# Optimization experiments

Measured on AMD Instinct MI355X. Metric: run time of the kernel, lower is better.

The kernel has to match this reference:

```python
import jax, jax.numpy as jnp
import numpy as np

N_WAY = 5
NKPTS = 17
EMBED = 512
N_SUPPORT = 25  # 5-way 5-shot
N_QUERY = 65536


def setup_inputs() -> dict:
    key = jax.random.key(0)
    ks = jax.random.split(key, 12)
    def lin(k, fan_in, fan_out):
        return jax.random.normal(k, (fan_in, fan_out), jnp.float32) / np.float32(np.sqrt(fan_in))
    return {
        'support_features': jax.random.normal(ks[0], (1, N_SUPPORT, EMBED), jnp.float32),
        'support_keypoints': jax.random.uniform(ks[1], (N_SUPPORT, NKPTS, 2), jnp.float32),
        'query_features': jax.random.normal(ks[2], (N_QUERY, EMBED), jnp.float32),
        'image_coords': jax.random.uniform(ks[3], (N_QUERY, 2), jnp.float32) * 512.0,
        'W1': lin(ks[4], EMBED, EMBED), 'b1': jnp.zeros((EMBED,), jnp.float32),
        'W2': lin(ks[5], EMBED, EMBED), 'b2': jnp.zeros((EMBED,), jnp.float32),
        'Wo1': lin(ks[6], EMBED, EMBED // 2), 'bo1': jnp.zeros((EMBED // 2,), jnp.float32),
        'Wo2': lin(ks[7], EMBED // 2, 2), 'bo2': jnp.zeros((2,), jnp.float32),
        'Wc1': lin(ks[8], EMBED, EMBED // 2), 'bc1': jnp.zeros((EMBED // 2,), jnp.float32),
        'Wc2': lin(ks[9], EMBED // 2, 1), 'bc2': jnp.zeros((1,), jnp.float32),
        'temperature': jnp.float32(1.0),
    }


def reference(support_features, support_keypoints, query_features, image_coords,
              W1, b1, W2, b2, Wo1, bo1, Wo2, bo2, Wc1, bc1, Wc2, bc2, temperature):
    eps = 1e-8
    nkpts = support_keypoints.shape[1]
    n_query = query_features.shape[0]
    D = query_features.shape[-1]

    # --- compute_prototypes (batch_size == 1; per-kpt prototype identical by construction) ---
    sf = support_features.reshape(-1, D)                      # [Ns, D]
    h = jnp.maximum(sf @ W1 + b1, 0.0) @ W2 + b2              # prototype_net MLP
    n_per = h.shape[0] // N_WAY
    proto_way = h.reshape(N_WAY, n_per, D).mean(axis=1)       # [n_way, D]
    prototypes = jnp.broadcast_to(proto_way[:, None, :], (N_WAY, nkpts, D))

    # --- compute_distances: 1 - cosine_sim, scaled by temperature ---
    qn = jnp.linalg.norm(query_features, axis=-1)             # [Nq]
    pn = jnp.linalg.norm(proto_way, axis=-1)                  # [n_way]
    sim = (query_features @ proto_way.T) / jnp.maximum(qn[:, None] * pn[None, :], eps)
    dist_way = (1.0 - sim) / temperature                      # [Nq, n_way]
    distances = jnp.broadcast_to(dist_way[:, :, None], (n_query, N_WAY, nkpts))

    # --- predict_keypoints ---
    # avg over kpts is a no-op (identical per kpt); argmin over ways
    class_predictions = jnp.argmin(dist_way, axis=1)          # [Nq] int
    # softmax over a single scalar == 1.0, so keypoints == offset broadcast over kpts
    offset = jnp.maximum(query_features @ Wo1 + bo1, 0.0) @ Wo2 + bo2   # [Nq, 2]
    conf = jax.nn.sigmoid(jnp.maximum(query_features @ Wc1 + bc1, 0.0) @ Wc2 + bc2)  # [Nq, 1]
    keypoints = jnp.broadcast_to(offset[:, None, :], (n_query, nkpts, 2))
    keypoints = jax.nn.sigmoid(keypoints) * image_coords[:, None, :]    # image_coords provided
    confidence = jnp.broadcast_to(conf, (n_query, nkpts))

    return keypoints, confidence, distances, class_predictions, prototypes
```

## Files before the change

### kernel.cpp

```cpp
#include <hip/hip_runtime.h>
#include <hip/hip_bf16.h>

#define NQ 65536
#define DIM 512
#define HID 256
#define NWAY 5
#define NKPTS 17
#define NS 25

typedef short bf16x8 __attribute__((ext_vector_type(8)));
typedef float f32x4 __attribute__((ext_vector_type(4)));
typedef _Float16 half8 __attribute__((ext_vector_type(8)));

static __device__ __forceinline__ unsigned short f2bf(float f) {
    unsigned int x = __float_as_uint(f);
    unsigned int r = (x + 0x7fffu + ((x >> 16) & 1u)) >> 16;
    return (unsigned short)r;
}

__global__ __launch_bounds__(256) void k_sup(const float* __restrict__ in,
                                             const float* __restrict__ W, const float* __restrict__ b,
                                             float* __restrict__ out, int relu) {
    int w = blockIdx.x * 4 + (threadIdx.x >> 6);
    int lane = threadIdx.x & 63;
    int s = w >> 9;
    int c = w & 511;
    const float* ip = in + s * DIM + lane * 8;
    float4 a0 = *(const float4*)ip;
    float4 a1 = *(const float4*)(ip + 4);
    float av[8] = {a0.x, a0.y, a0.z, a0.w, a1.x, a1.y, a1.z, a1.w};
    float acc = 0.0f;
    #pragma unroll
    for (int j = 0; j < 8; j++)
        acc += av[j] * W[(lane * 8 + j) * DIM + c];
    #pragma unroll
    for (int off = 32; off > 0; off >>= 1)
        acc += __shfl_xor(acc, off, 64);
    if (lane == 0) {
        float v = acc + b[c];
        out[s * DIM + c] = relu ? fmaxf(v, 0.0f) : v;
    }
}

__global__ __launch_bounds__(256) void k_proto(const float* __restrict__ ws_h,
                                               float* __restrict__ ws_proto, float* __restrict__ ws_pn,
                                               float* __restrict__ out_proto) {
    int w = blockIdx.x, t = threadIdx.x;
    __shared__ float s_p[DIM];
    __shared__ float red[256];
    for (int i = t; i < DIM; i += 256) {
        float a = 0.0f;
        for (int s = 0; s < 5; s++) a += ws_h[(w * 5 + s) * DIM + i];
        a *= 0.2f;
        s_p[i] = a;
        ws_proto[w * DIM + i] = a;
    }
    __syncthreads();
    float qq = 0.0f;
    for (int i = t; i < DIM; i += 256) qq += s_p[i] * s_p[i];
    red[t] = qq;
    __syncthreads();
    for (int s2 = 128; s2 > 0; s2 >>= 1) {
        if (t < s2) red[t] += red[t + s2];
        __syncthreads();
    }
    if (t == 0) ws_pn[w] = sqrtf(red[0]);
    for (int i = t; i < NKPTS * DIM; i += 256)
        out_proto[(size_t)w * NKPTS * DIM + i] = s_p[i & (DIM - 1)];
}

__global__ __launch_bounds__(256) void k_convw(const float* __restrict__ Wo1, const float* __restrict__ Wc1,
                                               unsigned short* __restrict__ wb) {
    int c = blockIdx.x;
    const float* src = (c < 256) ? Wo1 : Wc1;
    int cc = (c < 256) ? c : (c - 256);
    for (int k = threadIdx.x; k < DIM; k += 256)
        wb[c * DIM + k] = f2bf(src[k * HID + cc]);
}

__global__ __launch_bounds__(256, 2) void k_fused(const float* __restrict__ qf, const unsigned short* __restrict__ wb,
                                                  const float* __restrict__ ws_proto, const float* __restrict__ ws_pn,
                                                  const float* __restrict__ temp_p,
                                                  const float* __restrict__ bo1, const float* __restrict__ Wo2,
                                                  const float* __restrict__ bo2,
                                                  const float* __restrict__ bc1, const float* __restrict__ Wc2,
                                                  const float* __restrict__ bc2,
                                                  const float* __restrict__ ic,
                                                  float* __restrict__ out_kp, float* __restrict__ out_conf,
                                                  float* __restrict__ out_dist, float* __restrict__ out_class) {
    __shared__ __align__(16) char smem[37120];
    unsigned short* Alds = (unsigned short*)smem;
    unsigned short* Blds = (unsigned short*)(smem + 5120);
    float* s_proto = (float*)(smem + 25600);
    float* dlds = (float*)(smem + 35840);
    _Float16* hlds = (_Float16*)smem;
    float* offlds = (float*)(smem + 33792);

    int bx = blockIdx.x;
    int mb = bx >> 1;
    int nb = bx & 1;
    int t = threadIdx.x;
    int wv = t >> 6;
    int lane = t & 63;
    int r = lane & 15;
    int q8 = (lane >> 4) * 8;

    f32x4 acc[4][4];
    #pragma unroll
    for (int i = 0; i < 4; i++)
        #pragma unroll
        for (int j = 0; j < 4; j++) {
            f32x4 z = {0.0f, 0.0f, 0.0f, 0.0f};
            acc[i][j] = z;
        }

    int am = t >> 2;
    int akc = t & 3;
    const float* aptr = qf + ((size_t)(mb * 64 + am)) * DIM + akc * 8;
    const unsigned short* bptr = wb + ((size_t)(nb * 256 + t)) * DIM;

    if (nb == 0)
        for (int i = t; i < NWAY * DIM; i += 256) s_proto[i] = ws_proto[i];

    float ds[NWAY] = {0, 0, 0, 0, 0};
    float qq = 0.0f;

    float4 A0 = *(const float4*)(aptr);
    float4 A1 = *(const float4*)(aptr + 4);
    uint4 B0 = *(const uint4*)(bptr);
    uint4 B1 = *(const uint4*)(bptr + 8);
    uint4 B2 = *(const uint4*)(bptr + 16);
    uint4 B3 = *(const uint4*)(bptr + 24);

    for (int it = 0; it < 16; it++) {
        unsigned int p0 = f2bf(A0.x) | ((unsigned int)f2bf(A0.y) << 16);
        unsigned int p1 = f2bf(A0.z) | ((unsigned int)f2bf(A0.w) << 16);
        unsigned int p2 = f2bf(A1.x) | ((unsigned int)f2bf(A1.y) << 16);
        unsigned int p3 = f2bf(A1.z) | ((unsigned int)f2bf(A1.w) << 16);
        float av[8] = {A0.x, A0.y, A0.z, A0.w, A1.x, A1.y, A1.z, A1.w};
        __syncthreads();
        *(uint4*)(Alds + am * 40 + akc * 8) = make_uint4(p0, p1, p2, p3);
        *(uint4*)(Blds + t * 40) = B0;
        *(uint4*)(Blds + t * 40 + 8) = B1;
        *(uint4*)(Blds + t * 40 + 16) = B2;
        *(uint4*)(Blds + t * 40 + 24) = B3;
        __syncthreads();
        if (it < 15) {
            int k1 = (it + 1) * 32;
            A0 = *(const float4*)(aptr + k1);
            A1 = *(const float4*)(aptr + k1 + 4);
            B0 = *(const uint4*)(bptr + k1);
            B1 = *(const uint4*)(bptr + k1 + 8);
            B2 = *(const uint4*)(bptr + k1 + 16);
            B3 = *(const uint4*)(bptr + k1 + 24);
        }
        if (nb == 0) {
            int kb = it * 32 + akc * 8;
            #pragma unroll
            for (int w = 0; w < NWAY; w++) {
                f32x4 pv0 = *(const f32x4*)(s_proto + w * DIM + kb);
                f32x4 pv1 = *(const f32x4*)(s_proto + w * DIM + kb + 4);
                ds[w] += av[0] * pv0[0] + av[1] * pv0[1] + av[2] * pv0[2] + av[3] * pv0[3]
                       + av[4] * pv1[0] + av[5] * pv1[1] + av[6] * pv1[2] + av[7] * pv1[3];
            }
            #pragma unroll
            for (int j = 0; j < 8; j++) qq += av[j] * av[j];
        }
        bf16x8 af[4], bf[4];
        #pragma unroll
        for (int mt = 0; mt < 4; mt++)
            af[mt] = *(const bf16x8*)(Alds + (mt * 16 + r) * 40 + q8);
        #pragma unroll
        for (int nt = 0; nt < 4; nt++)
            bf[nt] = *(const bf16x8*)(Blds + (wv * 64 + nt * 16 + r) * 40 + q8);
        #pragma unroll
        for (int mt = 0; mt < 4; mt++)
            #pragma unroll
            for (int nt = 0; nt < 4; nt++)
                acc[mt][nt] = __builtin_amdgcn_mfma_f32_16x16x32_bf16(af[mt], bf[nt], acc[mt][nt], 0, 0, 0);
    }

    if (nb == 0) {
        #pragma unroll
        for (int off = 1; off <= 2; off <<= 1) {
            #pragma unroll
            for (int w = 0; w < NWAY; w++) ds[w] += __shfl_xor(ds[w], off, 64);
            qq += __shfl_xor(qq, off, 64);
        }
        if (akc == 0) {
            float qn = sqrtf(qq);
            float invt = 1.0f / temp_p[0];
            float mv = 1e30f;
            int ami = 0;
            #pragma unroll
            for (int w = 0; w < NWAY; w++) {
                float den = fmaxf(qn * ws_pn[w], 1e-8f);
                float d = (1.0f - ds[w] / den) * invt;
                dlds[am * 5 + w] = d;
                if (d < mv) { mv = d; ami = w; }
            }
            out_class[mb * 64 + am] = (float)ami;
        }
    }
    __syncthreads();
    if (nb == 0) {
        for (int i = t; i < 64 * NWAY * NKPTS; i += 256) {
            int q = i / (NWAY * NKPTS);
            int rem = i - q * (NWAY * NKPTS);
            out_dist[(size_t)(mb * 64 + q) * (NWAY * NKPTS) + rem] = dlds[q * 5 + rem / NKPTS];
        }
    }

    const float* bias = nb ? bc1 : bo1;
    #pragma unroll
    for (int nt = 0; nt < 4; nt++) {
        int cl = wv * 64 + nt * 16 + r;
        float bv = bias[cl];
        #pragma unroll
        for (int mt = 0; mt < 4; mt++)
            #pragma unroll
            for (int rg = 0; rg < 4; rg++) {
                int ml = mt * 16 + (lane >> 4) * 4 + rg;
                float v = acc[mt][nt][rg] + bv;
                hlds[ml * 264 + cl] = (_Float16)fmaxf(v, 0.0f);
            }
    }
    __syncthreads();

    if (nb == 0) {
        if (t < 64) {
            float ox = bo2[0], oy = bo2[1];
            for (int c0 = 0; c0 < 256; c0 += 8) {
                half8 hv = *(const half8*)(hlds + t * 264 + c0);
                #pragma unroll
                for (int j = 0; j < 8; j++) {
                    float hf = (float)hv[j];
                    ox += hf * Wo2[(c0 + j) * 2];
                    oy += hf * Wo2[(c0 + j) * 2 + 1];
                }
            }
            offlds[t * 2] = ox;
            offlds[t * 2 + 1] = oy;
        }
        __syncthreads();
        for (int i = t; i < 64 * 34; i += 256) {
            int q = i / 34;
            int rem = i - q * 34;
            int j = rem & 1;
            size_t Q = (size_t)mb * 64 + q;
            float o = offlds[q * 2 + j];
            float sg = 1.0f / (1.0f + __expf(-o));
            out_kp[Q * 34 + rem] = sg * ic[Q * 2 + j];
        }
    } else {
        if (t < 64) {
            float cl2 = bc2[0];
            for (int c0 = 0; c0 < 256; c0 += 8) {
                half8 hv = *(const half8*)(hlds + t * 264 + c0);
                #pragma unroll
                for (int j = 0; j < 8; j++) cl2 += (float)hv[j] * Wc2[c0 + j];
            }
            offlds[t] = 1.0f / (1.0f + __expf(-cl2));
        }
        __syncthreads();
        for (int i = t; i < 64 * 17; i += 256) {
            int q = i / 17;
            out_conf[(size_t)mb * 64 * 17 + i] = offlds[q];
        }
    }
}

extern "C" void kernel_launch(void* const* d_in, const int* in_sizes, int n_in,
                              void* d_out, int out_size, void* d_ws, size_t ws_size,
                              hipStream_t stream) {
    const float* sf = (const float*)d_in[0];
    const float* qf = (const float*)d_in[2];
    const float* ic = (const float*)d_in[3];
    const float* W1 = (const float*)d_in[4];
    const float* b1 = (const float*)d_in[5];
    const float* W2 = (const float*)d_in[6];
    const float* b2 = (const float*)d_in[7];
    const float* Wo1 = (const float*)d_in[8];
    const float* bo1 = (const float*)d_in[9];
    const float* Wo2 = (const float*)d_in[10];
    const float* bo2 = (const float*)d_in[11];
    const float* Wc1 = (const float*)d_in[12];
    const float* bc1 = (const float*)d_in[13];
    const float* Wc2 = (const float*)d_in[14];
    const float* bc2 = (const float*)d_in[15];
    const float* temp = (const float*)d_in[16];

    float* out = (float*)d_out;
    float* out_kp = out;
    float* out_conf = out + 2228224;
    float* out_dist = out + 3342336;
    float* out_class = out + 8912896;
    float* out_proto = out + 8978432;

    char* ws = (char*)d_ws;
    float* ws_h = (float*)ws;
    float* ws_proto = (float*)(ws + 51200);
    float* ws_pn = (float*)(ws + 61440);
    unsigned short* ws_wb = (unsigned short*)(ws + 65536);
    float* ws_h1 = (float*)(ws + 589824);

    hipLaunchKernelGGL(k_sup, dim3(3200), dim3(256), 0, stream, sf, W1, b1, ws_h1, 1);
    hipLaunchKernelGGL(k_sup, dim3(3200), dim3(256), 0, stream, ws_h1, W2, b2, ws_h, 0);
    hipLaunchKernelGGL(k_proto, dim3(5), dim3(256), 0, stream, ws_h, ws_proto, ws_pn, out_proto);
    hipLaunchKernelGGL(k_convw, dim3(512), dim3(256), 0, stream, Wo1, Wc1, ws_wb);
    hipLaunchKernelGGL(k_fused, dim3(2048), dim3(256), 0, stream, qf, ws_wb, ws_proto, ws_pn, temp,
                       bo1, Wo2, bo2, bc1, Wc2, bc2, ic, out_kp, out_conf, out_dist, out_class);
}
```

Measured before the change: 395.5 us.

## Fuse prototype mean into second support GEMM and split cosine work across blocks

Averages the support hidden activations before applying W2, using linearity, so the second support layer runs on 5 rows instead of 25. That layer is merged with a tiled LDS transpose/bf16 conversion of Wo1/Wc1 into one kernel, which cuts launches from five to three. The prototype-norm and prototype-broadcast kernel is removed: norms are recomputed inside the fused kernel and the prototype output is written by its first blocks. Cosine-distance work and distance output writes are now split between the two column blocks instead of all landing on nb==0. The launch_bounds occupancy hint of 2 is dropped, which may change register allocation.

```diff
diff --git a/kernel.cpp b/kernel.cpp
--- a/kernel.cpp
+++ b/kernel.cpp
@@ -6,7 +6,6 @@
 #define HID 256
 #define NWAY 5
 #define NKPTS 17
-#define NS 25
 
 typedef short bf16x8 __attribute__((ext_vector_type(8)));
 typedef float f32x4 __attribute__((ext_vector_type(4)));
@@ -18,81 +17,104 @@
     return (unsigned short)r;
 }
 
-__global__ __launch_bounds__(256) void k_sup(const float* __restrict__ in,
-                                             const float* __restrict__ W, const float* __restrict__ b,
-                                             float* __restrict__ out, int relu) {
+__global__ __launch_bounds__(256) void k_sup1(const float* __restrict__ sf,
+                                              const float* __restrict__ W1, const float* __restrict__ b1,
+                                              float* __restrict__ ws_h1) {
     int w = blockIdx.x * 4 + (threadIdx.x >> 6);
     int lane = threadIdx.x & 63;
     int s = w >> 9;
     int c = w & 511;
-    const float* ip = in + s * DIM + lane * 8;
+    const float* ip = sf + s * DIM + lane * 8;
     float4 a0 = *(const float4*)ip;
     float4 a1 = *(const float4*)(ip + 4);
     float av[8] = {a0.x, a0.y, a0.z, a0.w, a1.x, a1.y, a1.z, a1.w};
     float acc = 0.0f;
     #pragma unroll
     for (int j = 0; j < 8; j++)
-        acc += av[j] * W[(lane * 8 + j) * DIM + c];
+        acc += av[j] * W1[(lane * 8 + j) * DIM + c];
     #pragma unroll
     for (int off = 32; off > 0; off >>= 1)
         acc += __shfl_xor(acc, off, 64);
-    if (lane == 0) {
-        float v = acc + b[c];
-        out[s * DIM + c] = relu ? fmaxf(v, 0.0f) : v;
-    }
-}
-
-__global__ __launch_bounds__(256) void k_proto(const float* __restrict__ ws_h,
-                                               float* __restrict__ ws_proto, float* __restrict__ ws_pn,
+    if (lane == 0)
+        ws_h1[s * DIM + c] = fmaxf(acc + b1[c], 0.0f);
+}
+
+__global__ __launch_bounds__(256) void k_mid(const float* __restrict__ ws_h1,
+                                             const float* __restrict__ W2, const float* __restrict__ b2,
+                                             const float* __restrict__ Wo1, const float* __restrict__ Wc1,
+                                             float* __restrict__ ws_proto, unsigned short* __restrict__ wb) {
+    int bx = blockIdx.x;
+    int t = threadIdx.x;
+    if (bx < 640) {
+        int g = bx * 4 + (t >> 6);
+        int lane = t & 63;
+        int w = g >> 9;
+        int c = g & 511;
+        const float* base = ws_h1 + (w * 5) * DIM + lane * 8;
+        float av[8] = {0, 0, 0, 0, 0, 0, 0, 0};
+        #pragma unroll
+        for (int s = 0; s < 5; s++) {
+            float4 x0 = *(const float4*)(base + s * DIM);
+            float4 x1 = *(const float4*)(base + s * DIM + 4);
+            av[0] += x0.x; av[1] += x0.y; av[2] += x0.z; av[3] += x0.w;
+            av[4] += x1.x; av[5] += x1.y; av[6] += x1.z; av[7] += x1.w;
+        }
+        float acc = 0.0f;
+        #pragma unroll
+        for (int j = 0; j < 8; j++)
+            acc += (av[j] * 0.2f) * W2[(lane * 8 + j) * DIM + c];
+        #pragma unroll
+        for (int off = 32; off > 0; off >>= 1)
+            acc += __shfl_xor(acc, off, 64);
+        if (lane == 0)
+            ws_proto[w * DIM + c] = acc + b2[c];
+    } else {
+        __shared__ unsigned short T[64][72];
+        int tb = bx - 640;
+        const float* src = (tb < 32) ? Wo1 : Wc1;
+        int cofs = (tb < 32) ? 0 : 256;
+        int tt = tb & 31;
+        int kt = tt >> 2;
+        int ct = tt & 3;
+        int i = t >> 2;
+        int qd = t & 3;
+        const float* rp = src + (size_t)(kt * 64 + i) * HID + ct * 64 + qd * 16;
+        #pragma unroll
+        for (int v = 0; v < 4; v++) {
+            float4 x = *(const float4*)(rp + v * 4);
+            T[qd * 16 + v * 4 + 0][i] = f2bf(x.x);
+            T[qd * 16 + v * 4 + 1][i] = f2bf(x.y);
+            T[qd * 16 + v * 4 + 2][i] = f2bf(x.z);
+            T[qd * 16 + v * 4 + 3][i] = f2bf(x.w);
+        }
+        __syncthreads();
+        int j = t >> 2;
+        int part = t & 3;
+        uint4 o0 = *(const uint4*)&T[j][part * 16];
+        uint4 o1 = *(const uint4*)&T[j][part * 16 + 8];
+        unsigned short* dst = wb + (size_t)(cofs + ct * 64 + j) * DIM + kt * 64 + part * 16;
+        *(uint4*)dst = o0;
+        *(uint4*)(dst + 8) = o1;
+    }
+}
+
+__global__ __launch_bounds__(256) void k_fused(const float* __restrict__ qf, const unsigned short* __restrict__ wb,
+                                               const float* __restrict__ ws_proto,
+                                               const float* __restrict__ temp_p,
+                                               const float* __restrict__ bo1, const float* __restrict__ Wo2,
+                                               const float* __restrict__ bo2,
+                                               const float* __restrict__ bc1, const float* __restrict__ Wc2,
+                                               const float* __restrict__ bc2,
+                                               const float* __restrict__ ic,
+                                               float* __restrict__ out_kp, float* __restrict__ out_conf,
+                                               float* __restrict__ out_dist, float* __restrict__ out_class,
                                                float* __restrict__ out_proto) {
-    int w = blockIdx.x, t = threadIdx.x;
-    __shared__ float s_p[DIM];
-    __shared__ float red[256];
-    for (int i = t; i < DIM; i += 256) {
-        float a = 0.0f;
-        for (int s = 0; s < 5; s++) a += ws_h[(w * 5 + s) * DIM + i];
-        a *= 0.2f;
-        s_p[i] = a;
-        ws_proto[w * DIM + i] = a;
-    }
-    __syncthreads();
-    float qq = 0.0f;
-    for (int i = t; i < DIM; i += 256) qq += s_p[i] * s_p[i];
-    red[t] = qq;
-    __syncthreads();
-    for (int s2 = 128; s2 > 0; s2 >>= 1) {
-        if (t < s2) red[t] += red[t + s2];
-        __syncthreads();
-    }
-    if (t == 0) ws_pn[w] = sqrtf(red[0]);
-    for (int i = t; i < NKPTS * DIM; i += 256)
-        out_proto[(size_t)w * NKPTS * DIM + i] = s_p[i & (DIM - 1)];
-}
-
-__global__ __launch_bounds__(256) void k_convw(const float* __restrict__ Wo1, const float* __restrict__ Wc1,
-                                               unsigned short* __restrict__ wb) {
-    int c = blockIdx.x;
-    const float* src = (c < 256) ? Wo1 : Wc1;
-    int cc = (c < 256) ? c : (c - 256);
-    for (int k = threadIdx.x; k < DIM; k += 256)
-        wb[c * DIM + k] = f2bf(src[k * HID + cc]);
-}
-
-__global__ __launch_bounds__(256, 2) void k_fused(const float* __restrict__ qf, const unsigned short* __restrict__ wb,
-                                                  const float* __restrict__ ws_proto, const float* __restrict__ ws_pn,
-                                                  const float* __restrict__ temp_p,
-                                                  const float* __restrict__ bo1, const float* __restrict__ Wo2,
-                                                  const float* __restrict__ bo2,
-                                                  const float* __restrict__ bc1, const float* __restrict__ Wc2,
-                                                  const float* __restrict__ bc2,
-                                                  const float* __restrict__ ic,
-                                                  float* __restrict__ out_kp, float* __restrict__ out_conf,
-                                                  float* __restrict__ out_dist, float* __restrict__ out_class) {
-    __shared__ __align__(16) char smem[37120];
+    __shared__ __align__(16) char smem[37376];
     unsigned short* Alds = (unsigned short*)smem;
     unsigned short* Blds = (unsigned short*)(smem + 5120);
     float* s_proto = (float*)(smem + 25600);
     float* dlds = (float*)(smem + 35840);
+    float* pn_lds = (float*)(smem + 37120);
     _Float16* hlds = (_Float16*)smem;
     float* offlds = (float*)(smem + 33792);
 
@@ -105,6 +127,11 @@
     int r = lane & 15;
     int q8 = (lane >> 4) * 8;
 
+    if (bx < 85 && t < 128) {
+        f32x4 v = *(const f32x4*)(ws_proto + (bx / NKPTS) * DIM + t * 4);
+        *(f32x4*)(out_proto + (size_t)bx * DIM + t * 4) = v;
+    }
+
     f32x4 acc[4][4];
     #pragma unroll
     for (int i = 0; i < 4; i++)
@@ -116,11 +143,11 @@
 
     int am = t >> 2;
     int akc = t & 3;
+    int mine = ((t >> 7) == nb);
     const float* aptr = qf + ((size_t)(mb * 64 + am)) * DIM + akc * 8;
     const unsigned short* bptr = wb + ((size_t)(nb * 256 + t)) * DIM;
 
-    if (nb == 0)
-        for (int i = t; i < NWAY * DIM; i += 256) s_proto[i] = ws_proto[i];
+    for (int i = t; i < NWAY * DIM; i += 256) s_proto[i] = ws_proto[i];
 
     float ds[NWAY] = {0, 0, 0, 0, 0};
     float qq = 0.0f;
@@ -154,7 +181,7 @@
             B2 = *(const uint4*)(bptr + k1 + 16);
             B3 = *(const uint4*)(bptr + k1 + 24);
         }
-        if (nb == 0) {
+        if (mine) {
             int kb = it * 32 + akc * 8;
             #pragma unroll
             for (int w = 0; w < NWAY; w++) {
@@ -180,33 +207,45 @@
                 acc[mt][nt] = __builtin_amdgcn_mfma_f32_16x16x32_bf16(af[mt], bf[nt], acc[mt][nt], 0, 0, 0);
     }
 
-    if (nb == 0) {
+    for (int w = wv; w < NWAY; w += 4) {
+        f32x4 a = *(const f32x4*)(s_proto + w * DIM + lane * 8);
+        f32x4 b = *(const f32x4*)(s_proto + w * DIM + lane * 8 + 4);
+        float ss = a[0]*a[0] + a[1]*a[1] + a[2]*a[2] + a[3]*a[3]
+                 + b[0]*b[0] + b[1]*b[1] + b[2]*b[2] + b[3]*b[3];
+        #pragma unroll
+        for (int off = 32; off > 0; off >>= 1) ss += __shfl_xor(ss, off, 64);
+        if (lane == 0) pn_lds[w] = sqrtf(ss);
+    }
+    if (mine) {
         #pragma unroll
         for (int off = 1; off <= 2; off <<= 1) {
             #pragma unroll
             for (int w = 0; w < NWAY; w++) ds[w] += __shfl_xor(ds[w], off, 64);
             qq += __shfl_xor(qq, off, 64);
         }
-        if (akc == 0) {
-            float qn = sqrtf(qq);
-            float invt = 1.0f / temp_p[0];
-            float mv = 1e30f;
-            int ami = 0;
-            #pragma unroll
-            for (int w = 0; w < NWAY; w++) {
-                float den = fmaxf(qn * ws_pn[w], 1e-8f);
-                float d = (1.0f - ds[w] / den) * invt;
-                dlds[am * 5 + w] = d;
-                if (d < mv) { mv = d; ami = w; }
-            }
-            out_class[mb * 64 + am] = (float)ami;
-        }
     }
     __syncthreads();
-    if (nb == 0) {
-        for (int i = t; i < 64 * NWAY * NKPTS; i += 256) {
-            int q = i / (NWAY * NKPTS);
-            int rem = i - q * (NWAY * NKPTS);
+    if (mine && akc == 0) {
+        float qn = sqrtf(qq);
+        float invt = 1.0f / temp_p[0];
+        float mv = 1e30f;
+        int ami = 0;
+        #pragma unroll
+        for (int w = 0; w < NWAY; w++) {
+            float den = fmaxf(qn * pn_lds[w], 1e-8f);
+            float d = (1.0f - ds[w] / den) * invt;
+            dlds[am * 5 + w] = d;
+            if (d < mv) { mv = d; ami = w; }
+        }
+        out_class[mb * 64 + am] = (float)ami;
+    }
+    __syncthreads();
+
+    {
+        int qlo = nb * 32;
+        for (int i = t; i < 32 * NWAY * NKPTS; i += 256) {
+            int q = qlo + i / (NWAY * NKPTS);
+            int rem = i - (i / (NWAY * NKPTS)) * (NWAY * NKPTS);
             out_dist[(size_t)(mb * 64 + q) * (NWAY * NKPTS) + rem] = dlds[q * 5 + rem / NKPTS];
         }
     }
@@ -298,16 +337,12 @@
     float* out_proto = out + 8978432;
 
     char* ws = (char*)d_ws;
-    float* ws_h = (float*)ws;
+    float* ws_h1 = (float*)ws;
     float* ws_proto = (float*)(ws + 51200);
-    float* ws_pn = (float*)(ws + 61440);
     unsigned short* ws_wb = (unsigned short*)(ws + 65536);
-    float* ws_h1 = (float*)(ws + 589824);
-
-    hipLaunchKernelGGL(k_sup, dim3(3200), dim3(256), 0, stream, sf, W1, b1, ws_h1, 1);
-    hipLaunchKernelGGL(k_sup, dim3(3200), dim3(256), 0, stream, ws_h1, W2, b2, ws_h, 0);
-    hipLaunchKernelGGL(k_proto, dim3(5), dim3(256), 0, stream, ws_h, ws_proto, ws_pn, out_proto);
-    hipLaunchKernelGGL(k_convw, dim3(512), dim3(256), 0, stream, Wo1, Wc1, ws_wb);
-    hipLaunchKernelGGL(k_fused, dim3(2048), dim3(256), 0, stream, qf, ws_wb, ws_proto, ws_pn, temp,
-                       bo1, Wo2, bo2, bc1, Wc2, bc2, ic, out_kp, out_conf, out_dist, out_class);
-}
+
+    hipLaunchKernelGGL(k_sup1, dim3(3200), dim3(256), 0, stream, sf, W1, b1, ws_h1);
+    hipLaunchKernelGGL(k_mid, dim3(704), dim3(256), 0, stream, ws_h1, W2, b2, Wo1, Wc1, ws_proto, ws_wb);
+    hipLaunchKernelGGL(k_fused, dim3(2048), dim3(256), 0, stream, qf, ws_wb, ws_proto, temp,
+                       bo1, Wo2, bo2, bc1, Wc2, bc2, ic, out_kp, out_conf, out_dist, out_class, out_proto);
+}
```

New measurement: 366.1 us. 7.4% less time.
